# Performance work log

Hardware: AMD Instinct MI355X
Metric: run time of the kernel (lower is better)

## Reference

```python
import jax, jax.numpy as jnp
import numpy as np

LEAKY_SLOPE = 0.01  # torch nn.LeakyReLU default

def leaky_relu(x):
    return jnp.where(x >= 0, x, LEAKY_SLOPE * x)

def setup_inputs() -> dict:
    key = jax.random.key(0)
    ks = jax.random.split(key, 11)
    B, F, C_IN, H, K, D = 2048, 512, 3, 64, 8, 128  # batch, features, expand, layer_conf[0], bucket_num, bucket_dim
    ASR, MM, OUT = 128, 768, 256
    proj_in = ASR + MM + F * D
    inp = {
        "stat_features": jax.random.uniform(ks[0], (B, F), dtype=jnp.float32),
        "asr_embeddings": jax.random.normal(ks[1], (B, ASR), dtype=jnp.float32),
        "mm_embeddings": jax.random.normal(ks[2], (B, MM), dtype=jnp.float32),
        "linear1_w": jax.random.normal(ks[3], (F, C_IN, H), dtype=jnp.float32) * (1.0 / np.sqrt(C_IN)),
        "linear1_b": jax.random.normal(ks[4], (F, 1, H), dtype=jnp.float32),
        "linear2_w": jax.random.normal(ks[5], (F, H, K), dtype=jnp.float32) * (1.0 / np.sqrt(H)),
        "linear2_b": jax.random.normal(ks[6], (F, 1, K), dtype=jnp.float32),
        "tau": jnp.ones((F, 1, K), dtype=jnp.float32),
        "emb": jax.random.normal(ks[7], (F, K, D), dtype=jnp.float32),
        "proj_w": jax.random.normal(ks[8], (OUT, proj_in), dtype=jnp.float32) * (1.0 / np.sqrt(proj_in)),
        "proj_b": jax.random.normal(ks[9], (OUT,), dtype=jnp.float32) * 0.01,
    }
    return inp

def reference(stat_features, asr_embeddings, mm_embeddings,
              linear1_w, linear1_b, linear2_w, linear2_b, tau, emb,
              proj_w, proj_b):
    # sanitize: NaN -> 0, negatives -> 0
    x = stat_features
    x = jnp.where(jnp.isnan(x) | (x < 0.0), 0.0, x)  # [B, F]

    # auto_dis: per-feature tiny MLP. x is expanded to 3 identical copies -> [B,F,1,3]
    # matmul with [F,3,H] == einsum over the 3 copies.
    B, F = x.shape
    x3 = jnp.broadcast_to(x[:, :, None], (B, F, 3))           # [B,F,3]
    h = jnp.einsum('bfc,fch->bfh', x3, linear1_w) + linear1_b[:, 0, :]  # [B,F,H]
    h = jnp.where(h >= 0, h, LEAKY_SLOPE * h)
    s = jnp.einsum('bfh,fhk->bfk', h, linear2_w) + linear2_b[:, 0, :]   # [B,F,K]
    s = jnp.where(s >= 0, s, LEAKY_SLOPE * s)
    s = s * tau[:, 0, :]
    p = jax.nn.softmax(s, axis=-1)                            # [B,F,K]
    y = jnp.einsum('bfk,fkd->bfd', p, emb)                    # [B,F,D]
    y = y.reshape(B, -1)                                      # [B, F*D] (fc = Identity)

    z = jnp.concatenate([asr_embeddings, mm_embeddings, y], axis=1)
    out = jax.nn.relu(z @ proj_w.T + proj_b)                  # [B, 256]
    return out
```

## Files before the change

kernel.cpp:

```cpp
#include <hip/hip_runtime.h>
#include <hip/hip_bf16.h>
#include <math.h>

#define LEAKY 0.01f
#define B_    2048
#define F_    512
#define H_    64
#define K_    8
#define D_    128
#define ASR_  128
#define MM_   768
#define OUT_  256
#define PROJ_IN 66432
#define ZK    4992
#define PK    4096
#define NSPLIT 4


typedef unsigned short u16;
typedef u16   u16x4 __attribute__((ext_vector_type(4)));
typedef u16   u16x8 __attribute__((ext_vector_type(8)));
typedef short s16x8 __attribute__((ext_vector_type(8)));
typedef float f32x4 __attribute__((ext_vector_type(4)));

__device__ __forceinline__ u16 f2bf(float x) {
  unsigned int u = __float_as_uint(x);
  u += 0x7fffu + ((u >> 16) & 1u);
  return (u16)(u >> 16);
}

#define W1S 65
#define W2S 516
#define PRODUCER_BLOCKS (512 + 2048 + 224)

__global__ __launch_bounds__(256) void producer_kernel(
    const float* __restrict__ stat, const float* __restrict__ w1,
    const float* __restrict__ b1v, const float* __restrict__ w2,
    const float* __restrict__ b2v, const float* __restrict__ tauv,
    const float* __restrict__ pw, const float* __restrict__ emb,
    u16* __restrict__ P, u16* __restrict__ Wn) {
  __shared__ __align__(16) char smem[29376];
  const int bid = blockIdx.x;
  const int t = threadIdx.x;

  if (bid < 512) {
    const int f0 = (bid & 63) * 8;
    const int b0 = (bid >> 6) * 256;
    float* s_w1s = (float*)(smem);
    float* s_b1  = (float*)(smem + 2080);
    float* s_w2  = (float*)(smem + 4160);
    float* s_b2  = (float*)(smem + 20672);
    float* s_tau = (float*)(smem + 20928);
    float* s_x   = (float*)(smem + 21184);
    for (int i = t; i < 8 * 64; i += 256) {
      int fl = i >> 6, h = i & 63;
      const float* wf = w1 + (size_t)(f0 + fl) * 192;
      s_w1s[fl * W1S + h] = wf[h] + wf[64 + h] + wf[128 + h];
      s_b1[fl * W1S + h] = b1v[(size_t)(f0 + fl) * 64 + h];
    }
    for (int i = t; i < 8 * 512; i += 256) {
      int fl = i >> 9, idx = i & 511;
      s_w2[fl * W2S + idx] = w2[(size_t)(f0 + fl) * 512 + idx];
    }
    if (t < 64) {
      int fl = t >> 3, k = t & 7;
      s_b2[t]  = b2v[(f0 + fl) * 8 + k];
      s_tau[t] = tauv[(f0 + fl) * 8 + k];
    }
    for (int i = t; i < 2048; i += 256) {
      int r = i >> 3, j = i & 7;
      float v = stat[(size_t)(b0 + r) * F_ + f0 + j];
      s_x[i] = (v >= 0.f) ? v : 0.f;
    }
    __syncthreads();

    const int fl = t & 7, rb = t >> 3;
    float x[8];
    #pragma unroll
    for (int p = 0; p < 8; ++p) x[p] = s_x[(rb + 32 * p) * 8 + fl];
    float acc[8][8] = {{0.f}};
    const float* w1p = s_w1s + fl * W1S;
    const float* b1p = s_b1 + fl * W1S;
    const float* w2p = s_w2 + fl * W2S;
    #pragma unroll 8
    for (int i = 0; i < 64; ++i) {
      float wv = w1p[i], bv = b1p[i];
      float4 wa = *(const float4*)(w2p + i * 8);
      float4 wb = *(const float4*)(w2p + i * 8 + 4);
      #pragma unroll
      for (int p = 0; p < 8; ++p) {
        float h = fmaf(x[p], wv, bv);
        h = (h >= 0.f) ? h : LEAKY * h;
        acc[p][0] = fmaf(h, wa.x, acc[p][0]);
        acc[p][1] = fmaf(h, wa.y, acc[p][1]);
        acc[p][2] = fmaf(h, wa.z, acc[p][2]);
        acc[p][3] = fmaf(h, wa.w, acc[p][3]);
        acc[p][4] = fmaf(h, wb.x, acc[p][4]);
        acc[p][5] = fmaf(h, wb.y, acc[p][5]);
        acc[p][6] = fmaf(h, wb.z, acc[p][6]);
        acc[p][7] = fmaf(h, wb.w, acc[p][7]);
      }
    }
    #pragma unroll
    for (int p = 0; p < 8; ++p) {
      float s[K_];
      float m = -1e30f;
      #pragma unroll
      for (int k = 0; k < K_; ++k) {
        float v = acc[p][k] + s_b2[fl * 8 + k];
        v = (v >= 0.f) ? v : LEAKY * v;
        v *= s_tau[fl * 8 + k];
        s[k] = v;
        m = fmaxf(m, v);
      }
      float sum = 0.f;
      #pragma unroll
      for (int k = 0; k < K_; ++k) { s[k] = __expf(s[k] - m); sum += s[k]; }
      float inv = 1.f / sum;
      u16x8 hv;
      #pragma unroll
      for (int k = 0; k < K_; ++k) hv[k] = f2bf(s[k] * inv);
      *(u16x8*)(P + (size_t)(b0 + rb + 32 * p) * PK + (f0 + fl) * 8) = hv;
    }
  } else if (bid < 2560) {
    const int item = bid - 512;
    const int f = item >> 2;
    const int o0 = (item & 3) * 64;
    float* s_emb = (float*)smem;
    for (int i = t; i < K_ * D_; i += 256) s_emb[i] = emb[(size_t)f * K_ * D_ + i];
    __syncthreads();
    const int orow = t >> 2, dc = t & 3;
    const float* src = pw + (size_t)(o0 + orow) * PROJ_IN + 896 + f * D_;
    float g[K_] = {0.f, 0.f, 0.f, 0.f, 0.f, 0.f, 0.f, 0.f};
    #pragma unroll
    for (int j = 0; j < 8; ++j) {
      const int d = dc * 4 + j * 16;
      float4 w = *(const float4*)(src + d);
      #pragma unroll
      for (int k = 0; k < K_; ++k) {
        float4 e = *(const float4*)(s_emb + k * D_ + d);
        g[k] = fmaf(w.x, e.x, g[k]);
        g[k] = fmaf(w.y, e.y, g[k]);
        g[k] = fmaf(w.z, e.z, g[k]);
        g[k] = fmaf(w.w, e.w, g[k]);
      }
    }
    #pragma unroll
    for (int k = 0; k < K_; ++k) {
      g[k] += __shfl_xor(g[k], 1);
      g[k] += __shfl_xor(g[k], 2);
    }
    if (dc == 0) {
      u16x8 hv;
      #pragma unroll
      for (int k = 0; k < K_; ++k) hv[k] = f2bf(g[k]);
      *(u16x8*)(Wn + (size_t)(o0 + orow) * ZK + 896 + f * K_) = hv;
    }
  } else {
    const int item = bid - 2560;
    #pragma unroll
    for (int r = 0; r < 4; ++r) {
      int idx = item * 1024 + r * 256 + t;
      int o = idx / 896, j = idx % 896;
      Wn[(size_t)o * ZK + j] = f2bf(pw[(size_t)o * PROJ_IN + j]);
    }
  }
}

#define SAS 136
__global__ __launch_bounds__(256) void gemm_kernel(
    const float* __restrict__ asr, const float* __restrict__ mm,
    const u16* __restrict__ P, const u16* __restrict__ Wn,
    float* __restrict__ part) {
  const int bm0 = blockIdx.x * 32;
  const int bn0 = blockIdx.y * 32;
  const int kz  = blockIdx.z;
  const int it0 = kz * 10;
  const int itn = (kz == 3) ? 9 : 10;
  __shared__ u16 sA[32 * SAS];
  __shared__ u16 sB[32 * SAS];
  const int t = threadIdx.x;
  const int w = t >> 6, L = t & 63;
  const int l16 = L & 15, q8 = (L >> 4) * 8;
  const int mrow = (w >> 1) * 16, ncol = (w & 1) * 16;
  const int row = t >> 3, lk = t & 7;
  f32x4 acc = {0.f, 0.f, 0.f, 0.f};

  float4 fa[4];
  u16x8 pa[2];
  u16x8 wb[2];

#define LOAD_TILES(IT)                                                        \
  {                                                                           \
    const int k0_ = (IT) * 128;                                               \
    if (k0_ == 0) {                                                           \
      const float* s_ = asr + (size_t)(bm0 + row) * ASR_ + lk * 4;            \
      fa[0] = *(const float4*)(s_);                                           \
      fa[1] = *(const float4*)(s_ + 32);                                      \
      fa[2] = *(const float4*)(s_ + 64);                                      \
      fa[3] = *(const float4*)(s_ + 96);                                      \
    } else if (k0_ < 896) {                                                   \
      const float* s_ = mm + (size_t)(bm0 + row) * MM_ + (k0_ - 128) + lk * 4;\
      fa[0] = *(const float4*)(s_);                                           \
      fa[1] = *(const float4*)(s_ + 32);                                      \
      fa[2] = *(const float4*)(s_ + 64);                                      \
      fa[3] = *(const float4*)(s_ + 96);                                      \
    } else {                                                                  \
      const u16* s_ = P + (size_t)(bm0 + row) * PK + (k0_ - 896) + lk * 8;    \
      pa[0] = *(const u16x8*)(s_);                                            \
      pa[1] = *(const u16x8*)(s_ + 64);                                       \
    }                                                                         \
    const u16* sb_ = Wn + (size_t)(bn0 + row) * ZK + k0_ + lk * 8;            \
    wb[0] = *(const u16x8*)(sb_);                                             \
    wb[1] = *(const u16x8*)(sb_ + 64);                                        \
  }

#define STORE_TILES(IT)                                                       \
  {                                                                           \
    if ((IT) * 128 < 896) {                                                   \
      _Pragma("unroll")                                                       \
      for (int j_ = 0; j_ < 4; ++j_) {                                        \
        u16x4 h_ = {f2bf(fa[j_].x), f2bf(fa[j_].y), f2bf(fa[j_].z),           \
                    f2bf(fa[j_].w)};                                          \
        *(u16x4*)&sA[row * SAS + lk * 4 + j_ * 32] = h_;                      \
      }                                                                       \
    } else {                                                                  \
      *(u16x8*)&sA[row * SAS + lk * 8] = pa[0];                               \
      *(u16x8*)&sA[row * SAS + lk * 8 + 64] = pa[1];                          \
    }                                                                         \
    *(u16x8*)&sB[row * SAS + lk * 8] = wb[0];                                 \
    *(u16x8*)&sB[row * SAS + lk * 8 + 64] = wb[1];                            \
  }

  LOAD_TILES(it0);
  for (int it = it0; it < it0 + itn; ++it) {
    __syncthreads();
    STORE_TILES(it);
    __syncthreads();
    if (it + 1 < it0 + itn) LOAD_TILES(it + 1);
    #pragma unroll
    for (int ks = 0; ks < 4; ++ks) {
      s16x8 a = *(const s16x8*)&sA[(mrow + l16) * SAS + ks * 32 + q8];
      s16x8 b = *(const s16x8*)&sB[(ncol + l16) * SAS + ks * 32 + q8];
      acc = __builtin_amdgcn_mfma_f32_16x16x32_bf16(a, b, acc, 0, 0, 0);
    }
  }
#undef LOAD_TILES
#undef STORE_TILES

  const int col = bn0 + ncol + l16;
  const int r0 = bm0 + mrow + (L >> 4) * 4;
  float* dst = part + (size_t)kz * B_ * OUT_;
  #pragma unroll
  for (int i = 0; i < 4; ++i)
    dst[(size_t)(r0 + i) * OUT_ + col] = acc[i];
}

__global__ __launch_bounds__(256) void combine_kernel(
    const float* __restrict__ part, const float* __restrict__ pb,
    float* __restrict__ out) {
  const int idx4 = (blockIdx.x * 256 + threadIdx.x) * 4;
  const int o = idx4 & (OUT_ - 1);
  float4 a0 = *(const float4*)(part + idx4);
  float4 a1 = *(const float4*)(part + (size_t)B_ * OUT_ + idx4);
  float4 a2 = *(const float4*)(part + (size_t)2 * B_ * OUT_ + idx4);
  float4 a3 = *(const float4*)(part + (size_t)3 * B_ * OUT_ + idx4);
  float4 bv = *(const float4*)(pb + o);
  float4 r;
  r.x = a0.x + a1.x + a2.x + a3.x + bv.x;
  r.y = a0.y + a1.y + a2.y + a3.y + bv.y;
  r.z = a0.z + a1.z + a2.z + a3.z + bv.z;
  r.w = a0.w + a1.w + a2.w + a3.w + bv.w;
  r.x = r.x > 0.f ? r.x : 0.f;
  r.y = r.y > 0.f ? r.y : 0.f;
  r.z = r.z > 0.f ? r.z : 0.f;
  r.w = r.w > 0.f ? r.w : 0.f;
  *(float4*)(out + idx4) = r;
}

extern "C" void kernel_launch(void* const* d_in, const int* in_sizes, int n_in,
                              void* d_out, int out_size, void* d_ws, size_t ws_size,
                              hipStream_t stream) {
  (void)in_sizes; (void)n_in; (void)out_size; (void)ws_size;
  const float* stat = (const float*)d_in[0];
  const float* asr  = (const float*)d_in[1];
  const float* mm   = (const float*)d_in[2];
  const float* w1   = (const float*)d_in[3];
  const float* b1   = (const float*)d_in[4];
  const float* w2   = (const float*)d_in[5];
  const float* b2   = (const float*)d_in[6];
  const float* tau  = (const float*)d_in[7];
  const float* emb  = (const float*)d_in[8];
  const float* pw   = (const float*)d_in[9];
  const float* pb   = (const float*)d_in[10];
  float* out = (float*)d_out;
  char* ws = (char*)d_ws;
  u16*   P    = (u16*)(ws);
  u16*   Wn   = (u16*)(ws + 16777216);
  float* part = (float*)(ws + 19333120);

  producer_kernel<<<PRODUCER_BLOCKS, 256, 0, stream>>>(
      stat, w1, b1, w2, b2, tau, pw, emb, P, Wn);
  gemm_kernel<<<dim3(B_ / 32, OUT_ / 32, NSPLIT), 256, 0, stream>>>(
      asr, mm, P, Wn, part);
  combine_kernel<<<B_ * OUT_ / 1024, 256, 0, stream>>>(part, pb, out);
}
```

Baseline: 167.1 us.

## Enlarge GEMM tiles to 64x64 with 8-way split-K and halve producer feature tile

The GEMM block tile grows from 32x32 to 64x64, with each wave computing a 2x2 grid of MFMA fragments. This raises operand reuse from shared memory and cuts redundant global loads of A and B. Split-K goes from 4 to 8 so the grid stays large enough, at the cost of twice as many partial buffers written and then summed in the combine kernel. The producer's MLP stage now handles 4 features per block instead of 8, doubling the block count and halving shared memory and registers per block to improve occupancy.

```diff
diff --git a/kernel.cpp b/kernel.cpp
--- a/kernel.cpp
+++ b/kernel.cpp
@@ -14,7 +14,7 @@
 #define PROJ_IN 66432
 #define ZK    4992
 #define PK    4096
-#define NSPLIT 4
+#define NSPLIT 8
 
 
 typedef unsigned short u16;
@@ -31,7 +31,7 @@
 
 #define W1S 65
 #define W2S 516
-#define PRODUCER_BLOCKS (512 + 2048 + 224)
+#define PRODUCER_BLOCKS (1024 + 2048 + 224)
 
 __global__ __launch_bounds__(256) void producer_kernel(
     const float* __restrict__ stat, const float* __restrict__ w1,
@@ -39,46 +39,46 @@
     const float* __restrict__ b2v, const float* __restrict__ tauv,
     const float* __restrict__ pw, const float* __restrict__ emb,
     u16* __restrict__ P, u16* __restrict__ Wn) {
-  __shared__ __align__(16) char smem[29376];
+  __shared__ __align__(16) char smem[14688];
   const int bid = blockIdx.x;
   const int t = threadIdx.x;
 
-  if (bid < 512) {
-    const int f0 = (bid & 63) * 8;
-    const int b0 = (bid >> 6) * 256;
+  if (bid < 1024) {
+    const int f0 = (bid & 127) * 4;
+    const int b0 = (bid >> 7) * 256;
     float* s_w1s = (float*)(smem);
-    float* s_b1  = (float*)(smem + 2080);
-    float* s_w2  = (float*)(smem + 4160);
-    float* s_b2  = (float*)(smem + 20672);
-    float* s_tau = (float*)(smem + 20928);
-    float* s_x   = (float*)(smem + 21184);
-    for (int i = t; i < 8 * 64; i += 256) {
-      int fl = i >> 6, h = i & 63;
+    float* s_b1  = (float*)(smem + 1040);
+    float* s_w2  = (float*)(smem + 2080);
+    float* s_b2  = (float*)(smem + 10336);
+    float* s_tau = (float*)(smem + 10464);
+    float* s_x   = (float*)(smem + 10592);
+    {
+      int fl = t >> 6, h = t & 63;
       const float* wf = w1 + (size_t)(f0 + fl) * 192;
       s_w1s[fl * W1S + h] = wf[h] + wf[64 + h] + wf[128 + h];
       s_b1[fl * W1S + h] = b1v[(size_t)(f0 + fl) * 64 + h];
     }
-    for (int i = t; i < 8 * 512; i += 256) {
+    for (int i = t; i < 4 * 512; i += 256) {
       int fl = i >> 9, idx = i & 511;
       s_w2[fl * W2S + idx] = w2[(size_t)(f0 + fl) * 512 + idx];
     }
-    if (t < 64) {
+    if (t < 32) {
       int fl = t >> 3, k = t & 7;
       s_b2[t]  = b2v[(f0 + fl) * 8 + k];
       s_tau[t] = tauv[(f0 + fl) * 8 + k];
     }
-    for (int i = t; i < 2048; i += 256) {
-      int r = i >> 3, j = i & 7;
+    for (int i = t; i < 1024; i += 256) {
+      int r = i >> 2, j = i & 3;
       float v = stat[(size_t)(b0 + r) * F_ + f0 + j];
       s_x[i] = (v >= 0.f) ? v : 0.f;
     }
     __syncthreads();
 
-    const int fl = t & 7, rb = t >> 3;
-    float x[8];
-    #pragma unroll
-    for (int p = 0; p < 8; ++p) x[p] = s_x[(rb + 32 * p) * 8 + fl];
-    float acc[8][8] = {{0.f}};
+    const int fl = t & 3, rb = t >> 2;
+    float x[4];
+    #pragma unroll
+    for (int p = 0; p < 4; ++p) x[p] = s_x[(rb + 64 * p) * 4 + fl];
+    float acc[4][8] = {{0.f}};
     const float* w1p = s_w1s + fl * W1S;
     const float* b1p = s_b1 + fl * W1S;
     const float* w2p = s_w2 + fl * W2S;
@@ -88,7 +88,7 @@
       float4 wa = *(const float4*)(w2p + i * 8);
       float4 wb = *(const float4*)(w2p + i * 8 + 4);
       #pragma unroll
-      for (int p = 0; p < 8; ++p) {
+      for (int p = 0; p < 4; ++p) {
         float h = fmaf(x[p], wv, bv);
         h = (h >= 0.f) ? h : LEAKY * h;
         acc[p][0] = fmaf(h, wa.x, acc[p][0]);
@@ -102,7 +102,7 @@
       }
     }
     #pragma unroll
-    for (int p = 0; p < 8; ++p) {
+    for (int p = 0; p < 4; ++p) {
       float s[K_];
       float m = -1e30f;
       #pragma unroll
@@ -120,10 +120,10 @@
       u16x8 hv;
       #pragma unroll
       for (int k = 0; k < K_; ++k) hv[k] = f2bf(s[k] * inv);
-      *(u16x8*)(P + (size_t)(b0 + rb + 32 * p) * PK + (f0 + fl) * 8) = hv;
-    }
-  } else if (bid < 2560) {
-    const int item = bid - 512;
+      *(u16x8*)(P + (size_t)(b0 + rb + 64 * p) * PK + (f0 + fl) * 8) = hv;
+    }
+  } else if (bid < 3072) {
+    const int item = bid - 1024;
     const int f = item >> 2;
     const int o0 = (item & 3) * 64;
     float* s_emb = (float*)smem;
@@ -157,7 +157,7 @@
       *(u16x8*)(Wn + (size_t)(o0 + orow) * ZK + 896 + f * K_) = hv;
     }
   } else {
-    const int item = bid - 2560;
+    const int item = bid - 3072;
     #pragma unroll
     for (int r = 0; r < 4; ++r) {
       int idx = item * 1024 + r * 256 + t;
@@ -172,64 +172,62 @@
     const float* __restrict__ asr, const float* __restrict__ mm,
     const u16* __restrict__ P, const u16* __restrict__ Wn,
     float* __restrict__ part) {
-  const int bm0 = blockIdx.x * 32;
-  const int bn0 = blockIdx.y * 32;
+  const int bm0 = blockIdx.x * 64;
+  const int bn0 = blockIdx.y * 64;
   const int kz  = blockIdx.z;
-  const int it0 = kz * 10;
-  const int itn = (kz == 3) ? 9 : 10;
-  __shared__ u16 sA[32 * SAS];
-  __shared__ u16 sB[32 * SAS];
+  const int it0 = kz * 5;
+  const int itn = (kz == 7) ? 4 : 5;
+  __shared__ u16 sA[64 * SAS];
+  __shared__ u16 sB[64 * SAS];
   const int t = threadIdx.x;
   const int w = t >> 6, L = t & 63;
   const int l16 = L & 15, q8 = (L >> 4) * 8;
-  const int mrow = (w >> 1) * 16, ncol = (w & 1) * 16;
-  const int row = t >> 3, lk = t & 7;
-  f32x4 acc = {0.f, 0.f, 0.f, 0.f};
-
-  float4 fa[4];
-  u16x8 pa[2];
-  u16x8 wb[2];
+  const int wm = (w >> 1) * 32, wn = (w & 1) * 32;
+  const int row = t >> 2, lk = t & 3;
+  f32x4 acc[2][2] = {{{0.f,0.f,0.f,0.f},{0.f,0.f,0.f,0.f}},
+                     {{0.f,0.f,0.f,0.f},{0.f,0.f,0.f,0.f}}};
+  float4 fa[8];
+  u16x8 pa[4];
+  u16x8 wb[4];
 
 #define LOAD_TILES(IT)                                                        \
   {                                                                           \
     const int k0_ = (IT) * 128;                                               \
     if (k0_ == 0) {                                                           \
-      const float* s_ = asr + (size_t)(bm0 + row) * ASR_ + lk * 4;            \
-      fa[0] = *(const float4*)(s_);                                           \
-      fa[1] = *(const float4*)(s_ + 32);                                      \
-      fa[2] = *(const float4*)(s_ + 64);                                      \
-      fa[3] = *(const float4*)(s_ + 96);                                      \
+      const float* s_ = asr + (size_t)(bm0 + row) * ASR_ + lk * 32;           \
+      _Pragma("unroll")                                                       \
+      for (int j_ = 0; j_ < 8; ++j_) fa[j_] = *(const float4*)(s_ + j_ * 4);  \
     } else if (k0_ < 896) {                                                   \
-      const float* s_ = mm + (size_t)(bm0 + row) * MM_ + (k0_ - 128) + lk * 4;\
-      fa[0] = *(const float4*)(s_);                                           \
-      fa[1] = *(const float4*)(s_ + 32);                                      \
-      fa[2] = *(const float4*)(s_ + 64);                                      \
-      fa[3] = *(const float4*)(s_ + 96);                                      \
+      const float* s_ = mm + (size_t)(bm0 + row) * MM_ + (k0_ - 128) + lk * 32;\
+      _Pragma("unroll")                                                       \
+      for (int j_ = 0; j_ < 8; ++j_) fa[j_] = *(const float4*)(s_ + j_ * 4);  \
     } else {                                                                  \
-      const u16* s_ = P + (size_t)(bm0 + row) * PK + (k0_ - 896) + lk * 8;    \
-      pa[0] = *(const u16x8*)(s_);                                            \
-      pa[1] = *(const u16x8*)(s_ + 64);                                       \
+      const u16* s_ = P + (size_t)(bm0 + row) * PK + (k0_ - 896) + lk * 32;   \
+      _Pragma("unroll")                                                       \
+      for (int j_ = 0; j_ < 4; ++j_) pa[j_] = *(const u16x8*)(s_ + j_ * 8);   \
     }                                                                         \
-    const u16* sb_ = Wn + (size_t)(bn0 + row) * ZK + k0_ + lk * 8;            \
-    wb[0] = *(const u16x8*)(sb_);                                             \
-    wb[1] = *(const u16x8*)(sb_ + 64);                                        \
+    const u16* sb_ = Wn + (size_t)(bn0 + row) * ZK + k0_ + lk * 32;           \
+    _Pragma("unroll")                                                         \
+    for (int j_ = 0; j_ < 4; ++j_) wb[j_] = *(const u16x8*)(sb_ + j_ * 8);    \
   }
 
 #define STORE_TILES(IT)                                                       \
   {                                                                           \
     if ((IT) * 128 < 896) {                                                   \
       _Pragma("unroll")                                                       \
-      for (int j_ = 0; j_ < 4; ++j_) {                                        \
+      for (int j_ = 0; j_ < 8; ++j_) {                                        \
         u16x4 h_ = {f2bf(fa[j_].x), f2bf(fa[j_].y), f2bf(fa[j_].z),           \
                     f2bf(fa[j_].w)};                                          \
-        *(u16x4*)&sA[row * SAS + lk * 4 + j_ * 32] = h_;                      \
+        *(u16x4*)&sA[row * SAS + lk * 32 + j_ * 4] = h_;                      \
       }                                                                       \
     } else {                                                                  \
-      *(u16x8*)&sA[row * SAS + lk * 8] = pa[0];                               \
-      *(u16x8*)&sA[row * SAS + lk * 8 + 64] = pa[1];                          \
+      _Pragma("unroll")                                                       \
+      for (int j_ = 0; j_ < 4; ++j_)                                          \
+        *(u16x8*)&sA[row * SAS + lk * 32 + j_ * 8] = pa[j_];                  \
     }                                                                         \
-    *(u16x8*)&sB[row * SAS + lk * 8] = wb[0];                                 \
-    *(u16x8*)&sB[row * SAS + lk * 8 + 64] = wb[1];                            \
+    _Pragma("unroll")                                                         \
+    for (int j_ = 0; j_ < 4; ++j_)                                            \
+      *(u16x8*)&sB[row * SAS + lk * 32 + j_ * 8] = wb[j_];                    \
   }
 
   LOAD_TILES(it0);
@@ -240,20 +238,31 @@
     if (it + 1 < it0 + itn) LOAD_TILES(it + 1);
     #pragma unroll
     for (int ks = 0; ks < 4; ++ks) {
-      s16x8 a = *(const s16x8*)&sA[(mrow + l16) * SAS + ks * 32 + q8];
-      s16x8 b = *(const s16x8*)&sB[(ncol + l16) * SAS + ks * 32 + q8];
-      acc = __builtin_amdgcn_mfma_f32_16x16x32_bf16(a, b, acc, 0, 0, 0);
+      s16x8 a0 = *(const s16x8*)&sA[(wm + l16) * SAS + ks * 32 + q8];
+      s16x8 a1 = *(const s16x8*)&sA[(wm + 16 + l16) * SAS + ks * 32 + q8];
+      s16x8 b0 = *(const s16x8*)&sB[(wn + l16) * SAS + ks * 32 + q8];
+      s16x8 b1 = *(const s16x8*)&sB[(wn + 16 + l16) * SAS + ks * 32 + q8];
+      acc[0][0] = __builtin_amdgcn_mfma_f32_16x16x32_bf16(a0, b0, acc[0][0], 0, 0, 0);
+      acc[0][1] = __builtin_amdgcn_mfma_f32_16x16x32_bf16(a0, b1, acc[0][1], 0, 0, 0);
+      acc[1][0] = __builtin_amdgcn_mfma_f32_16x16x32_bf16(a1, b0, acc[1][0], 0, 0, 0);
+      acc[1][1] = __builtin_amdgcn_mfma_f32_16x16x32_bf16(a1, b1, acc[1][1], 0, 0, 0);
     }
   }
 #undef LOAD_TILES
 #undef STORE_TILES
 
-  const int col = bn0 + ncol + l16;
-  const int r0 = bm0 + mrow + (L >> 4) * 4;
   float* dst = part + (size_t)kz * B_ * OUT_;
   #pragma unroll
-  for (int i = 0; i < 4; ++i)
-    dst[(size_t)(r0 + i) * OUT_ + col] = acc[i];
+  for (int mf = 0; mf < 2; ++mf) {
+    const int r0 = bm0 + wm + mf * 16 + (L >> 4) * 4;
+    #pragma unroll
+    for (int nf = 0; nf < 2; ++nf) {
+      const int col = bn0 + wn + nf * 16 + l16;
+      #pragma unroll
+      for (int i = 0; i < 4; ++i)
+        dst[(size_t)(r0 + i) * OUT_ + col] = acc[mf][nf][i];
+    }
+  }
 }
 
 __global__ __launch_bounds__(256) void combine_kernel(
@@ -261,16 +270,13 @@
     float* __restrict__ out) {
   const int idx4 = (blockIdx.x * 256 + threadIdx.x) * 4;
   const int o = idx4 & (OUT_ - 1);
-  float4 a0 = *(const float4*)(part + idx4);
-  float4 a1 = *(const float4*)(part + (size_t)B_ * OUT_ + idx4);
-  float4 a2 = *(const float4*)(part + (size_t)2 * B_ * OUT_ + idx4);
-  float4 a3 = *(const float4*)(part + (size_t)3 * B_ * OUT_ + idx4);
   float4 bv = *(const float4*)(pb + o);
-  float4 r;
-  r.x = a0.x + a1.x + a2.x + a3.x + bv.x;
-  r.y = a0.y + a1.y + a2.y + a3.y + bv.y;
-  r.z = a0.z + a1.z + a2.z + a3.z + bv.z;
-  r.w = a0.w + a1.w + a2.w + a3.w + bv.w;
+  float4 r = bv;
+  #pragma unroll
+  for (int kz = 0; kz < NSPLIT; ++kz) {
+    float4 a = *(const float4*)(part + (size_t)kz * B_ * OUT_ + idx4);
+    r.x += a.x; r.y += a.y; r.z += a.z; r.w += a.w;
+  }
   r.x = r.x > 0.f ? r.x : 0.f;
   r.y = r.y > 0.f ? r.y : 0.f;
   r.z = r.z > 0.f ? r.z : 0.f;
@@ -301,7 +307,7 @@
 
   producer_kernel<<<PRODUCER_BLOCKS, 256, 0, stream>>>(
       stat, w1, b1, w2, b2, tau, pw, emb, P, Wn);
-  gemm_kernel<<<dim3(B_ / 32, OUT_ / 32, NSPLIT), 256, 0, stream>>>(
+  gemm_kernel<<<dim3(B_ / 64, OUT_ / 64, NSPLIT), 256, 0, stream>>>(
       asr, mm, P, Wn, part);
   combine_kernel<<<B_ * OUT_ / 1024, 256, 0, stream>>>(part, pb, out);
 }
```

Result: slower. 171.5 us (+2.6%).
